# Optimization experiments

Measured on AMD Instinct MI355X. Metric: run time of the kernel, lower is better.

Reference implementation:

```python
import jax, jax.numpy as jnp
import numpy as np

NEG_FILL = -999999.0  # sentinel used by the original torch code when masking a channel


def setup_inputs() -> dict:
    key = jax.random.key(0)
    M = jax.random.normal(key, (64, 512, 28, 28), dtype=jnp.float32)
    return {"M": M}


def _dis_loss(M):
    # M: (b, c, h, w). Squared distance from each pixel to the per-map argmax, weighted by M.
    b, c, h, w = M.shape
    Mm = M.reshape(b * c, h, w)
    ind = jnp.argmax(Mm.reshape(b * c, h * w), axis=1)  # flat argmax per map
    indy = ind // w
    indx = ind % w
    y = jnp.arange(h)
    x = jnp.arange(w)
    dy2 = (indy[:, None, None] - y[None, :, None]) ** 2  # (bc, h, 1)
    dx2 = (indx[:, None, None] - x[None, None, :]) ** 2  # (bc, 1, w)
    dist_sq = (dy2 + dx2).astype(M.dtype)  # (bc, h, w)
    return jnp.mean(dist_sq * Mm)


def _div_loss(M):
    # Leave-one-out channel max times each channel, via a single top-2 over channels
    # (equivalent to the O(C^2) clone+max loop in the original).
    b, c, h, w = M.shape
    Mt = jnp.transpose(M, (0, 2, 3, 1))  # (b, h, w, c)
    vals, idxs = jax.lax.top_k(Mt, 2)    # (b, h, w, 2)
    ch = jnp.arange(c)
    # loo[..., c] = max over channels != c
    loo = jnp.where(ch[None, None, None, :] == idxs[..., :1], vals[..., 1:2], vals[..., :1])
    # Original caps the masked channel at -999999; only matters if all other channels < -999999.
    loo = jnp.maximum(loo, NEG_FILL)
    return jnp.mean(loo * Mt)


def reference(M):
    dis_loss = _dis_loss(M)
    div_loss = _div_loss(M)
    return (dis_loss, div_loss)
```

## Files before the change

### kernel.cpp

```cpp
#include <hip/hip_runtime.h>
#include <math.h>

#define BB 64
#define CC 512
#define HWP 784
#define NPIX4 12544
#define NCHUNK 16
#define NSLOTS 512
#define NEG_FILL -999999.0f
#define NTOT 25690112.0
#define PLANE_STRIDE 200704

static __device__ __forceinline__ unsigned sortable(float v) {
  unsigned b = __float_as_uint(v);
  return (b & 0x80000000u) ? ~b : (b | 0x80000000u);
}

static __device__ __forceinline__ void top2(float v, float& v1, float& v2) {
  float lo = fminf(v, v1);
  v1 = fmaxf(v1, v);
  v2 = fmaxf(v2, lo);
}

static __device__ __forceinline__ void mergev(float& v1, float& v2, float b1, float b2) {
  float lo = fminf(v1, b1);
  v1 = fmaxf(v1, b1);
  v2 = fmaxf(lo, fmaxf(v2, b2));
}
static __device__ __forceinline__ void mergev4(float4& v1, float4& v2, float4 b1, float4 b2) {
  mergev(v1.x, v2.x, b1.x, b2.x);
  mergev(v1.y, v2.y, b1.y, b2.y);
  mergev(v1.z, v2.z, b1.z, b2.z);
  mergev(v1.w, v2.w, b1.w, b2.w);
}

__global__ __launch_bounds__(256, 4) void fused_kernel(const float* __restrict__ M,
    double* __restrict__ slots, float4* __restrict__ wsV1,
    float4* __restrict__ wsV2, float4* __restrict__ wsS) {
  const int lane  = threadIdx.x & 63;
  const int w     = threadIdx.x >> 6;
  const int chunk = blockIdx.x;
  const int b     = blockIdx.y;
  const float* base = M + ((size_t)b * CC + chunk * 32 + w * 8) * HWP;

  float s0[8], sy[8], sx[8], bv[8];
  int bi[8];
  #pragma unroll
  for (int c = 0; c < 8; ++c) { s0[c]=0.f; sy[c]=0.f; sx[c]=0.f; bv[c]=-INFINITY; bi[c]=0; }
  float srr = 0.f;

  __shared__ float4 lm[4][3][196];

  auto process = [&](int f) {
    const int y  = f / 7;
    const int x0 = (f - y * 7) * 4;
    const float fy  = (float)y;
    const float fx0 = (float)x0, fx1 = fx0 + 1.f, fx2 = fx0 + 2.f, fx3 = fx0 + 3.f;
    const float fyy = fy * fy;
    const float rr0 = fyy + fx0*fx0, rr1 = fyy + fx1*fx1;
    const float rr2 = fyy + fx2*fx2, rr3 = fyy + fx3*fx3;
    const int pxb = f * 4;

    float4 d[8];
    #pragma unroll
    for (int c = 0; c < 8; ++c)
      d[c] = *(const float4*)(base + c * HWP + pxb);

    const float NI = -INFINITY;
    float4 v1 = make_float4(NI, NI, NI, NI);
    float4 v2 = v1;
    float4 S  = make_float4(0.f, 0.f, 0.f, 0.f);

    #pragma unroll
    for (int c = 0; c < 8; ++c) {
      const float a0 = d[c].x, a1 = d[c].y, a2 = d[c].z, a3 = d[c].w;
      const float sum4 = (a0 + a1) + (a2 + a3);
      s0[c] += sum4;
      sy[c] = fmaf(sum4, fy, sy[c]);
      sx[c] = fmaf(a0, fx0, sx[c]); sx[c] = fmaf(a1, fx1, sx[c]);
      sx[c] = fmaf(a2, fx2, sx[c]); sx[c] = fmaf(a3, fx3, sx[c]);
      srr = fmaf(a0, rr0, srr); srr = fmaf(a1, rr1, srr);
      srr = fmaf(a2, rr2, srr); srr = fmaf(a3, rr3, srr);
      if (a0 > bv[c]) { bv[c] = a0; bi[c] = pxb;     }
      if (a1 > bv[c]) { bv[c] = a1; bi[c] = pxb + 1; }
      if (a2 > bv[c]) { bv[c] = a2; bi[c] = pxb + 2; }
      if (a3 > bv[c]) { bv[c] = a3; bi[c] = pxb + 3; }
      top2(a0, v1.x, v2.x); S.x += a0;
      top2(a1, v1.y, v2.y); S.y += a1;
      top2(a2, v1.z, v2.z); S.z += a2;
      top2(a3, v1.w, v2.w); S.w += a3;
    }
    lm[w][0][f] = v1; lm[w][1][f] = v2; lm[w][2][f] = S;
  };

  #pragma unroll
  for (int k = 0; k < 3; ++k) process(lane + 64 * k);
  if (lane < 4) process(192 + lane);

  double dis_acc = (double)srr;
  #pragma unroll
  for (int c = 0; c < 8; ++c) {
    unsigned long long key =
        ((unsigned long long)sortable(bv[c]) << 32) | (unsigned)(~bi[c]);
    #pragma unroll
    for (int off = 1; off < 64; off <<= 1) {
      unsigned long long o = __shfl_xor(key, off);
      key = (key > o) ? key : o;
    }
    const int px = (int)(~((unsigned)key));
    const int iy = px / 28;
    const int ix = px - iy * 28;
    dis_acc += (double)s0[c] * (double)(iy * iy + ix * ix)
             - 2.0 * ((double)sy[c] * (double)iy + (double)sx[c] * (double)ix);
  }
  #pragma unroll
  for (int off = 32; off >= 1; off >>= 1)
    dis_acc += __shfl_down(dis_acc, off);
  if (lane == 0)
    atomicAdd(&slots[(((b * NCHUNK) + chunk) * 4 + w) & (NSLOTS - 1)], dis_acc);

  __syncthreads();
  const int t = threadIdx.x;
  if (t < 196) {
    float4 mv1 = lm[0][0][t], mv2 = lm[0][1][t], mS = lm[0][2][t];
    #pragma unroll
    for (int ww = 1; ww < 4; ++ww) {
      mergev4(mv1, mv2, lm[ww][0][t], lm[ww][1][t]);
      float4 bS = lm[ww][2][t];
      mS.x += bS.x; mS.y += bS.y; mS.z += bS.z; mS.w += bS.w;
    }
    const int idx = chunk * NPIX4 + b * 196 + t;
    wsV1[idx] = mv1; wsV2[idx] = mv2; wsS[idx] = mS;
  }
}

__global__ __launch_bounds__(256) void div_merge_kernel(const float4* __restrict__ wsV1,
    const float4* __restrict__ wsV2, const float4* __restrict__ wsS,
    double* __restrict__ slots) {
  const int t = threadIdx.x, lane = t & 63, w = t >> 6;
  const int g = blockIdx.x * 64 + lane;

  float4 a1[4], a2[4], aS[4];
  #pragma unroll
  for (int c = 0; c < 4; ++c) {
    const int idx = (w * 4 + c) * NPIX4 + g;
    a1[c] = wsV1[idx]; a2[c] = wsV2[idx]; aS[c] = wsS[idx];
  }
  float4 v1 = a1[0], v2 = a2[0], S = aS[0];
  #pragma unroll
  for (int c = 1; c < 4; ++c) {
    mergev4(v1, v2, a1[c], a2[c]);
    S.x += aS[c].x; S.y += aS[c].y; S.z += aS[c].z; S.w += aS[c].w;
  }
  __shared__ float4 sm[4][3][64];
  sm[w][0][lane] = v1; sm[w][1][lane] = v2; sm[w][2][lane] = S;
  __syncthreads();

  if (t < 64) {
    v1 = sm[0][0][t]; v2 = sm[0][1][t]; S = sm[0][2][t];
    #pragma unroll
    for (int ww = 1; ww < 4; ++ww) {
      mergev4(v1, v2, sm[ww][0][t], sm[ww][1][t]);
      float4 bS = sm[ww][2][t];
      S.x += bS.x; S.y += bS.y; S.z += bS.z; S.w += bS.w;
    }
    double contrib =
        (double)fmaxf(v1.x, NEG_FILL) * ((double)S.x - (double)v1.x) + (double)fmaxf(v2.x, NEG_FILL) * (double)v1.x
      + (double)fmaxf(v1.y, NEG_FILL) * ((double)S.y - (double)v1.y) + (double)fmaxf(v2.y, NEG_FILL) * (double)v1.y
      + (double)fmaxf(v1.z, NEG_FILL) * ((double)S.z - (double)v1.z) + (double)fmaxf(v2.z, NEG_FILL) * (double)v1.z
      + (double)fmaxf(v1.w, NEG_FILL) * ((double)S.w - (double)v1.w) + (double)fmaxf(v2.w, NEG_FILL) * (double)v1.w;
    #pragma unroll
    for (int off = 32; off >= 1; off >>= 1)
      contrib += __shfl_down(contrib, off);
    if (t == 0)
      atomicAdd(&slots[NSLOTS + blockIdx.x], contrib);
  }
}

__global__ __launch_bounds__(512) void finalize_kernel(const double* __restrict__ slots,
                                                       float* __restrict__ out) {
  const int t = threadIdx.x;
  const int lane = t & 63, wave = t >> 6;
  double dis = slots[t];
  double dv  = slots[NSLOTS + t];
  #pragma unroll
  for (int off = 32; off >= 1; off >>= 1) {
    dis += __shfl_down(dis, off);
    dv  += __shfl_down(dv,  off);
  }
  __shared__ double pd[8], pv[8];
  if (lane == 0) { pd[wave] = dis; pv[wave] = dv; }
  __syncthreads();
  if (t == 0) {
    double D = 0.0, V = 0.0;
    #pragma unroll
    for (int i = 0; i < 8; ++i) { D += pd[i]; V += pv[i]; }
    out[0] = (float)(D / NTOT);
    out[1] = (float)(V / NTOT);
  }
}

extern "C" void kernel_launch(void* const* d_in, const int* in_sizes, int n_in,
                              void* d_out, int out_size, void* d_ws, size_t ws_size,
                              hipStream_t stream) {
  const float* M = (const float*)d_in[0];
  double* slots = (double*)d_ws;
  float4* planes = (float4*)((char*)d_ws + 16384);
  hipMemsetAsync(d_ws, 0, 2 * NSLOTS * sizeof(double), stream);
  fused_kernel<<<dim3(NCHUNK, BB), 256, 0, stream>>>(
      M, slots, planes, planes + PLANE_STRIDE, planes + 2 * PLANE_STRIDE);
  div_merge_kernel<<<196, 256, 0, stream>>>(
      planes, planes + PLANE_STRIDE, planes + 2 * PLANE_STRIDE, slots);
  finalize_kernel<<<1, 512, 0, stream>>>(slots, (float*)d_out);
}
```

Measured before the change: 43.38 us.

## Use float2 loads with register double-buffering and drop atomics and memset

The main kernel now loads float2 instead of float4 per lane and software-pipelines the loads, fetching the next chunk of 8 channel rows into a second register set while the current one is processed. The tail is handled by a masked pass. The atomicAdd accumulation into hashed slots is replaced by a direct per-wave store into dedicated slots, which removes the hipMemsetAsync launch, and the finalize kernel sums the larger slot array. The intent is better memory-latency hiding and less launch and atomic overhead, at the cost of higher register pressure and more, smaller loads.

```diff
diff --git a/kernel.cpp b/kernel.cpp
--- a/kernel.cpp
+++ b/kernel.cpp
@@ -4,44 +4,40 @@
 #define BB 64
 #define CC 512
 #define HWP 784
+#define NF2 392
+#define NCHUNK 16
 #define NPIX4 12544
-#define NCHUNK 16
-#define NSLOTS 512
+#define NPIX2 25088
+#define PLANE2 401408
+#define DIS_SLOTS 4096
+#define DIV_SLOTS 196
 #define NEG_FILL -999999.0f
 #define NTOT 25690112.0
-#define PLANE_STRIDE 200704
 
 static __device__ __forceinline__ unsigned sortable(float v) {
   unsigned b = __float_as_uint(v);
   return (b & 0x80000000u) ? ~b : (b | 0x80000000u);
 }
-
 static __device__ __forceinline__ void top2(float v, float& v1, float& v2) {
   float lo = fminf(v, v1);
   v1 = fmaxf(v1, v);
   v2 = fmaxf(v2, lo);
 }
-
 static __device__ __forceinline__ void mergev(float& v1, float& v2, float b1, float b2) {
   float lo = fminf(v1, b1);
   v1 = fmaxf(v1, b1);
   v2 = fmaxf(lo, fmaxf(v2, b2));
 }
-static __device__ __forceinline__ void mergev4(float4& v1, float4& v2, float4 b1, float4 b2) {
-  mergev(v1.x, v2.x, b1.x, b2.x);
-  mergev(v1.y, v2.y, b1.y, b2.y);
-  mergev(v1.z, v2.z, b1.z, b2.z);
-  mergev(v1.w, v2.w, b1.w, b2.w);
-}
 
 __global__ __launch_bounds__(256, 4) void fused_kernel(const float* __restrict__ M,
-    double* __restrict__ slots, float4* __restrict__ wsV1,
-    float4* __restrict__ wsV2, float4* __restrict__ wsS) {
+    double* __restrict__ slots, float2* __restrict__ wsV1,
+    float2* __restrict__ wsV2, float2* __restrict__ wsS) {
   const int lane  = threadIdx.x & 63;
   const int w     = threadIdx.x >> 6;
   const int chunk = blockIdx.x;
   const int b     = blockIdx.y;
-  const float* base = M + ((size_t)b * CC + chunk * 32 + w * 8) * HWP;
+  const float2* base2 =
+      (const float2*)(M + ((size_t)b * CC + chunk * 32 + w * 8) * HWP);
 
   float s0[8], sy[8], sx[8], bv[8];
   int bi[8];
@@ -49,53 +45,58 @@
   for (int c = 0; c < 8; ++c) { s0[c]=0.f; sy[c]=0.f; sx[c]=0.f; bv[c]=-INFINITY; bi[c]=0; }
   float srr = 0.f;
 
-  __shared__ float4 lm[4][3][196];
-
-  auto process = [&](int f) {
-    const int y  = f / 7;
-    const int x0 = (f - y * 7) * 4;
+  __shared__ float2 lm[4][3][NF2];
+
+  float2 d[8], dn[8];
+  const int f2m = (lane < 8) ? (384 + lane) : 390;
+
+  #pragma unroll
+  for (int c = 0; c < 8; ++c) d[c] = base2[c * NF2 + lane];
+
+  auto consume = [&](int f2pos, bool masked) {
+    const int y  = f2pos / 14;
+    const int x0 = (f2pos - y * 14) * 2;
     const float fy  = (float)y;
-    const float fx0 = (float)x0, fx1 = fx0 + 1.f, fx2 = fx0 + 2.f, fx3 = fx0 + 3.f;
+    const float fx0 = (float)x0, fx1 = fx0 + 1.f;
     const float fyy = fy * fy;
-    const float rr0 = fyy + fx0*fx0, rr1 = fyy + fx1*fx1;
-    const float rr2 = fyy + fx2*fx2, rr3 = fyy + fx3*fx3;
-    const int pxb = f * 4;
-
-    float4 d[8];
-    #pragma unroll
-    for (int c = 0; c < 8; ++c)
-      d[c] = *(const float4*)(base + c * HWP + pxb);
-
-    const float NI = -INFINITY;
-    float4 v1 = make_float4(NI, NI, NI, NI);
-    float4 v2 = v1;
-    float4 S  = make_float4(0.f, 0.f, 0.f, 0.f);
-
+    const float rr0 = fyy + fx0 * fx0, rr1 = fyy + fx1 * fx1;
+    const int pxb = f2pos * 2;
+    const bool fake = masked && (lane >= 8);
+
+    float v1a = -INFINITY, v2a = -INFINITY, Sa = 0.f;
+    float v1b = -INFINITY, v2b = -INFINITY, Sb = 0.f;
     #pragma unroll
     for (int c = 0; c < 8; ++c) {
-      const float a0 = d[c].x, a1 = d[c].y, a2 = d[c].z, a3 = d[c].w;
-      const float sum4 = (a0 + a1) + (a2 + a3);
-      s0[c] += sum4;
-      sy[c] = fmaf(sum4, fy, sy[c]);
+      float a0 = d[c].x, a1 = d[c].y;
+      float c0 = a0,     c1 = a1;
+      if (masked && fake) { a0 = 0.f; a1 = 0.f; c0 = -INFINITY; c1 = -INFINITY; }
+      const float sum2 = a0 + a1;
+      s0[c] += sum2;
+      sy[c] = fmaf(sum2, fy, sy[c]);
       sx[c] = fmaf(a0, fx0, sx[c]); sx[c] = fmaf(a1, fx1, sx[c]);
-      sx[c] = fmaf(a2, fx2, sx[c]); sx[c] = fmaf(a3, fx3, sx[c]);
-      srr = fmaf(a0, rr0, srr); srr = fmaf(a1, rr1, srr);
-      srr = fmaf(a2, rr2, srr); srr = fmaf(a3, rr3, srr);
-      if (a0 > bv[c]) { bv[c] = a0; bi[c] = pxb;     }
-      if (a1 > bv[c]) { bv[c] = a1; bi[c] = pxb + 1; }
-      if (a2 > bv[c]) { bv[c] = a2; bi[c] = pxb + 2; }
-      if (a3 > bv[c]) { bv[c] = a3; bi[c] = pxb + 3; }
-      top2(a0, v1.x, v2.x); S.x += a0;
-      top2(a1, v1.y, v2.y); S.y += a1;
-      top2(a2, v1.z, v2.z); S.z += a2;
-      top2(a3, v1.w, v2.w); S.w += a3;
-    }
-    lm[w][0][f] = v1; lm[w][1][f] = v2; lm[w][2][f] = S;
+      srr   = fmaf(a0, rr0, srr);   srr   = fmaf(a1, rr1, srr);
+      if (c0 > bv[c]) { bv[c] = c0; bi[c] = pxb;     }
+      if (c1 > bv[c]) { bv[c] = c1; bi[c] = pxb + 1; }
+      top2(c0, v1a, v2a); Sa += a0;
+      top2(c1, v1b, v2b); Sb += a1;
+    }
+    if (!masked || lane < 8) {
+      lm[w][0][f2pos] = make_float2(v1a, v1b);
+      lm[w][1][f2pos] = make_float2(v2a, v2b);
+      lm[w][2][f2pos] = make_float2(Sa, Sb);
+    }
   };
 
   #pragma unroll
-  for (int k = 0; k < 3; ++k) process(lane + 64 * k);
-  if (lane < 4) process(192 + lane);
+  for (int k = 0; k < 6; ++k) {
+    const int nf2 = (k == 5) ? f2m : (lane + 64 * (k + 1));
+    #pragma unroll
+    for (int c = 0; c < 8; ++c) dn[c] = base2[c * NF2 + nf2];
+    consume(lane + 64 * k, false);
+    #pragma unroll
+    for (int c = 0; c < 8; ++c) d[c] = dn[c];
+  }
+  consume(384 + lane, true);
 
   double dis_acc = (double)srr;
   #pragma unroll
@@ -117,20 +118,25 @@
   for (int off = 32; off >= 1; off >>= 1)
     dis_acc += __shfl_down(dis_acc, off);
   if (lane == 0)
-    atomicAdd(&slots[(((b * NCHUNK) + chunk) * 4 + w) & (NSLOTS - 1)], dis_acc);
+    slots[((b * NCHUNK + chunk) << 2) | w] = dis_acc;
 
   __syncthreads();
   const int t = threadIdx.x;
-  if (t < 196) {
-    float4 mv1 = lm[0][0][t], mv2 = lm[0][1][t], mS = lm[0][2][t];
-    #pragma unroll
-    for (int ww = 1; ww < 4; ++ww) {
-      mergev4(mv1, mv2, lm[ww][0][t], lm[ww][1][t]);
-      float4 bS = lm[ww][2][t];
-      mS.x += bS.x; mS.y += bS.y; mS.z += bS.z; mS.w += bS.w;
-    }
-    const int idx = chunk * NPIX4 + b * 196 + t;
-    wsV1[idx] = mv1; wsV2[idx] = mv2; wsS[idx] = mS;
+  #pragma unroll
+  for (int rep = 0; rep < 2; ++rep) {
+    const int f = t + rep * 256;
+    if (f < NF2) {
+      float2 mv1 = lm[0][0][f], mv2 = lm[0][1][f], mS = lm[0][2][f];
+      #pragma unroll
+      for (int ww = 1; ww < 4; ++ww) {
+        float2 b1 = lm[ww][0][f], b2 = lm[ww][1][f], bS = lm[ww][2][f];
+        mergev(mv1.x, mv2.x, b1.x, b2.x);
+        mergev(mv1.y, mv2.y, b1.y, b2.y);
+        mS.x += bS.x; mS.y += bS.y;
+      }
+      const int idx = chunk * NPIX2 + b * NF2 + f;
+      wsV1[idx] = mv1; wsV2[idx] = mv2; wsS[idx] = mS;
+    }
   }
 }
 
@@ -149,7 +155,10 @@
   float4 v1 = a1[0], v2 = a2[0], S = aS[0];
   #pragma unroll
   for (int c = 1; c < 4; ++c) {
-    mergev4(v1, v2, a1[c], a2[c]);
+    mergev(v1.x, v2.x, a1[c].x, a2[c].x);
+    mergev(v1.y, v2.y, a1[c].y, a2[c].y);
+    mergev(v1.z, v2.z, a1[c].z, a2[c].z);
+    mergev(v1.w, v2.w, a1[c].w, a2[c].w);
     S.x += aS[c].x; S.y += aS[c].y; S.z += aS[c].z; S.w += aS[c].w;
   }
   __shared__ float4 sm[4][3][64];
@@ -160,7 +169,10 @@
     v1 = sm[0][0][t]; v2 = sm[0][1][t]; S = sm[0][2][t];
     #pragma unroll
     for (int ww = 1; ww < 4; ++ww) {
-      mergev4(v1, v2, sm[ww][0][t], sm[ww][1][t]);
+      mergev(v1.x, v2.x, sm[ww][0][t].x, sm[ww][1][t].x);
+      mergev(v1.y, v2.y, sm[ww][0][t].y, sm[ww][1][t].y);
+      mergev(v1.z, v2.z, sm[ww][0][t].z, sm[ww][1][t].z);
+      mergev(v1.w, v2.w, sm[ww][0][t].w, sm[ww][1][t].w);
       float4 bS = sm[ww][2][t];
       S.x += bS.x; S.y += bS.y; S.z += bS.z; S.w += bS.w;
     }
@@ -173,30 +185,28 @@
     for (int off = 32; off >= 1; off >>= 1)
       contrib += __shfl_down(contrib, off);
     if (t == 0)
-      atomicAdd(&slots[NSLOTS + blockIdx.x], contrib);
-  }
-}
-
-__global__ __launch_bounds__(512) void finalize_kernel(const double* __restrict__ slots,
+      slots[DIS_SLOTS + blockIdx.x] = contrib;
+  }
+}
+
+__global__ __launch_bounds__(256) void finalize_kernel(const double* __restrict__ slots,
                                                        float* __restrict__ out) {
-  const int t = threadIdx.x;
-  const int lane = t & 63, wave = t >> 6;
-  double dis = slots[t];
-  double dv  = slots[NSLOTS + t];
+  const int t = threadIdx.x, lane = t & 63, wv = t >> 6;
+  double dis = 0.0;
+  #pragma unroll
+  for (int i = 0; i < 16; ++i) dis += slots[t + (i << 8)];
+  double dv = (t < DIV_SLOTS) ? slots[DIS_SLOTS + t] : 0.0;
   #pragma unroll
   for (int off = 32; off >= 1; off >>= 1) {
     dis += __shfl_down(dis, off);
     dv  += __shfl_down(dv,  off);
   }
-  __shared__ double pd[8], pv[8];
-  if (lane == 0) { pd[wave] = dis; pv[wave] = dv; }
+  __shared__ double pd[4], pv[4];
+  if (lane == 0) { pd[wv] = dis; pv[wv] = dv; }
   __syncthreads();
   if (t == 0) {
-    double D = 0.0, V = 0.0;
-    #pragma unroll
-    for (int i = 0; i < 8; ++i) { D += pd[i]; V += pv[i]; }
-    out[0] = (float)(D / NTOT);
-    out[1] = (float)(V / NTOT);
+    out[0] = (float)((pd[0] + pd[1] + pd[2] + pd[3]) / NTOT);
+    out[1] = (float)((pv[0] + pv[1] + pv[2] + pv[3]) / NTOT);
   }
 }
 
@@ -205,11 +215,12 @@
                               hipStream_t stream) {
   const float* M = (const float*)d_in[0];
   double* slots = (double*)d_ws;
-  float4* planes = (float4*)((char*)d_ws + 16384);
-  hipMemsetAsync(d_ws, 0, 2 * NSLOTS * sizeof(double), stream);
-  fused_kernel<<<dim3(NCHUNK, BB), 256, 0, stream>>>(
-      M, slots, planes, planes + PLANE_STRIDE, planes + 2 * PLANE_STRIDE);
-  div_merge_kernel<<<196, 256, 0, stream>>>(
-      planes, planes + PLANE_STRIDE, planes + 2 * PLANE_STRIDE, slots);
-  finalize_kernel<<<1, 512, 0, stream>>>(slots, (float*)d_out);
-}
+  float2* planes = (float2*)((char*)d_ws + 65536);
+  float2* wsV1 = planes;
+  float2* wsV2 = planes + PLANE2;
+  float2* wsS  = planes + 2 * (size_t)PLANE2;
+  fused_kernel<<<dim3(NCHUNK, BB), 256, 0, stream>>>(M, slots, wsV1, wsV2, wsS);
+  div_merge_kernel<<<DIV_SLOTS, 256, 0, stream>>>(
+      (const float4*)wsV1, (const float4*)wsV2, (const float4*)wsS, slots);
+  finalize_kernel<<<1, 256, 0, stream>>>(slots, (float*)d_out);
+}
```

Result: slower. 45.56 us (+5.0%).

## Software-pipeline channel loads and fold finalize into merge via last-block ticket

Applied to the files above, without the earlier changes.

The main kernel now prefetches the next pixel group's channel data in two halves while computing the current one. The ragged tail lanes run the same code path with masked fake values, which removes divergence. The memset and the separate finalize kernel are gone: per-wave partials are written to unique slots instead of atomically added, and the last div_merge block, chosen by an atomic ticket counter, does the final reduction. This cuts two launches and adds more register pressure and a threadfence/atomic handshake.

```diff
diff --git a/kernel.cpp b/kernel.cpp
--- a/kernel.cpp
+++ b/kernel.cpp
@@ -4,24 +4,24 @@
 #define BB 64
 #define CC 512
 #define HWP 784
+#define NF4 196
+#define NCHUNK 16
 #define NPIX4 12544
-#define NCHUNK 16
-#define NSLOTS 512
+#define PLANE4 200704
+#define DIS_SLOTS 4096
+#define DIV_SLOTS 196
 #define NEG_FILL -999999.0f
 #define NTOT 25690112.0
-#define PLANE_STRIDE 200704
 
 static __device__ __forceinline__ unsigned sortable(float v) {
   unsigned b = __float_as_uint(v);
   return (b & 0x80000000u) ? ~b : (b | 0x80000000u);
 }
-
 static __device__ __forceinline__ void top2(float v, float& v1, float& v2) {
   float lo = fminf(v, v1);
   v1 = fmaxf(v1, v);
   v2 = fmaxf(v2, lo);
 }
-
 static __device__ __forceinline__ void mergev(float& v1, float& v2, float b1, float b2) {
   float lo = fminf(v1, b1);
   v1 = fmaxf(v1, b1);
@@ -34,14 +34,48 @@
   mergev(v1.w, v2.w, b1.w, b2.w);
 }
 
+#define CHBODY(c) {                                                          \
+    float a0 = d[c].x, a1 = d[c].y, a2 = d[c].z, a3 = d[c].w;                \
+    float q0 = a0, q1 = a1, q2 = a2, q3 = a3;                                \
+    if (fake) { a0 = a1 = a2 = a3 = 0.f;                                     \
+                q0 = q1 = q2 = q3 = -INFINITY; }                             \
+    const float sum4 = (a0 + a1) + (a2 + a3);                                \
+    s0[c] += sum4;                                                           \
+    sy[c] = fmaf(sum4, fy, sy[c]);                                           \
+    sx[c] = fmaf(a0, fx0, sx[c]); sx[c] = fmaf(a1, fx1, sx[c]);              \
+    sx[c] = fmaf(a2, fx2, sx[c]); sx[c] = fmaf(a3, fx3, sx[c]);              \
+    srr = fmaf(a0, rr0, srr); srr = fmaf(a1, rr1, srr);                      \
+    srr = fmaf(a2, rr2, srr); srr = fmaf(a3, rr3, srr);                      \
+    if (q0 > bv[c]) { bv[c] = q0; bi[c] = pxb;     }                         \
+    if (q1 > bv[c]) { bv[c] = q1; bi[c] = pxb + 1; }                         \
+    if (q2 > bv[c]) { bv[c] = q2; bi[c] = pxb + 2; }                         \
+    if (q3 > bv[c]) { bv[c] = q3; bi[c] = pxb + 3; }                         \
+    top2(q0, v1.x, v2.x); S.x += a0;                                         \
+    top2(q1, v1.y, v2.y); S.y += a1;                                         \
+    top2(q2, v1.z, v2.z); S.z += a2;                                         \
+    top2(q3, v1.w, v2.w); S.w += a3; }
+
+#define GEOM(f)                                                              \
+    const int y = (f) / 7;                                                   \
+    const float fy  = (float)y;                                              \
+    const float fx0 = (float)(((f) - y * 7) * 4);                            \
+    const float fx1 = fx0 + 1.f, fx2 = fx0 + 2.f, fx3 = fx0 + 3.f;           \
+    const float fyy = fy * fy;                                               \
+    const float rr0 = fyy + fx0 * fx0, rr1 = fyy + fx1 * fx1;                \
+    const float rr2 = fyy + fx2 * fx2, rr3 = fyy + fx3 * fx3;                \
+    const int pxb = (f) * 4;
+
 __global__ __launch_bounds__(256, 4) void fused_kernel(const float* __restrict__ M,
-    double* __restrict__ slots, float4* __restrict__ wsV1,
-    float4* __restrict__ wsV2, float4* __restrict__ wsS) {
+    double* __restrict__ slots, float4* __restrict__ wsV1, float4* __restrict__ wsV2,
+    float4* __restrict__ wsS, unsigned* __restrict__ counter) {
   const int lane  = threadIdx.x & 63;
   const int w     = threadIdx.x >> 6;
   const int chunk = blockIdx.x;
   const int b     = blockIdx.y;
-  const float* base = M + ((size_t)b * CC + chunk * 32 + w * 8) * HWP;
+  if (chunk == 0 && b == 0 && threadIdx.x == 0) *counter = 0u;
+
+  const float4* base4 =
+      (const float4*)(M + ((size_t)b * CC + chunk * 32 + w * 8) * HWP);
 
   float s0[8], sy[8], sx[8], bv[8];
   int bi[8];
@@ -49,53 +83,44 @@
   for (int c = 0; c < 8; ++c) { s0[c]=0.f; sy[c]=0.f; sx[c]=0.f; bv[c]=-INFINITY; bi[c]=0; }
   float srr = 0.f;
 
-  __shared__ float4 lm[4][3][196];
-
-  auto process = [&](int f) {
-    const int y  = f / 7;
-    const int x0 = (f - y * 7) * 4;
-    const float fy  = (float)y;
-    const float fx0 = (float)x0, fx1 = fx0 + 1.f, fx2 = fx0 + 2.f, fx3 = fx0 + 3.f;
-    const float fyy = fy * fy;
-    const float rr0 = fyy + fx0*fx0, rr1 = fyy + fx1*fx1;
-    const float rr2 = fyy + fx2*fx2, rr3 = fyy + fx3*fx3;
-    const int pxb = f * 4;
-
-    float4 d[8];
-    #pragma unroll
-    for (int c = 0; c < 8; ++c)
-      d[c] = *(const float4*)(base + c * HWP + pxb);
-
-    const float NI = -INFINITY;
-    float4 v1 = make_float4(NI, NI, NI, NI);
+  __shared__ float4 lm[4][3][NF4];
+
+  float4 d[8], dn[4];
+  #pragma unroll
+  for (int c = 0; c < 8; ++c) d[c] = base4[c * NF4 + lane];
+
+  const int tailf = (lane < 4) ? (192 + lane) : 195;
+
+  #pragma unroll
+  for (int k = 0; k < 3; ++k) {
+    const int f  = lane + 64 * k;
+    const int nf = (k == 2) ? tailf : (lane + 64 * (k + 1));
+    const bool fake = false;
+    GEOM(f)
+    float4 v1 = make_float4(-INFINITY, -INFINITY, -INFINITY, -INFINITY);
     float4 v2 = v1;
     float4 S  = make_float4(0.f, 0.f, 0.f, 0.f);
-
-    #pragma unroll
-    for (int c = 0; c < 8; ++c) {
-      const float a0 = d[c].x, a1 = d[c].y, a2 = d[c].z, a3 = d[c].w;
-      const float sum4 = (a0 + a1) + (a2 + a3);
-      s0[c] += sum4;
-      sy[c] = fmaf(sum4, fy, sy[c]);
-      sx[c] = fmaf(a0, fx0, sx[c]); sx[c] = fmaf(a1, fx1, sx[c]);
-      sx[c] = fmaf(a2, fx2, sx[c]); sx[c] = fmaf(a3, fx3, sx[c]);
-      srr = fmaf(a0, rr0, srr); srr = fmaf(a1, rr1, srr);
-      srr = fmaf(a2, rr2, srr); srr = fmaf(a3, rr3, srr);
-      if (a0 > bv[c]) { bv[c] = a0; bi[c] = pxb;     }
-      if (a1 > bv[c]) { bv[c] = a1; bi[c] = pxb + 1; }
-      if (a2 > bv[c]) { bv[c] = a2; bi[c] = pxb + 2; }
-      if (a3 > bv[c]) { bv[c] = a3; bi[c] = pxb + 3; }
-      top2(a0, v1.x, v2.x); S.x += a0;
-      top2(a1, v1.y, v2.y); S.y += a1;
-      top2(a2, v1.z, v2.z); S.z += a2;
-      top2(a3, v1.w, v2.w); S.w += a3;
-    }
+    #pragma unroll
+    for (int c = 0; c < 4; ++c) dn[c] = base4[c * NF4 + nf];
+    CHBODY(4) CHBODY(5) CHBODY(6) CHBODY(7)
+    #pragma unroll
+    for (int c = 4; c < 8; ++c) d[c] = base4[c * NF4 + nf];
+    CHBODY(0) CHBODY(1) CHBODY(2) CHBODY(3)
+    #pragma unroll
+    for (int c = 0; c < 4; ++c) d[c] = dn[c];
     lm[w][0][f] = v1; lm[w][1][f] = v2; lm[w][2][f] = S;
-  };
-
-  #pragma unroll
-  for (int k = 0; k < 3; ++k) process(lane + 64 * k);
-  if (lane < 4) process(192 + lane);
+  }
+  {
+    const int f = tailf;
+    const bool fake = (lane >= 4);
+    GEOM(f)
+    float4 v1 = make_float4(-INFINITY, -INFINITY, -INFINITY, -INFINITY);
+    float4 v2 = v1;
+    float4 S  = make_float4(0.f, 0.f, 0.f, 0.f);
+    CHBODY(0) CHBODY(1) CHBODY(2) CHBODY(3)
+    CHBODY(4) CHBODY(5) CHBODY(6) CHBODY(7)
+    if (!fake) { lm[w][0][f] = v1; lm[w][1][f] = v2; lm[w][2][f] = S; }
+  }
 
   double dis_acc = (double)srr;
   #pragma unroll
@@ -117,11 +142,11 @@
   for (int off = 32; off >= 1; off >>= 1)
     dis_acc += __shfl_down(dis_acc, off);
   if (lane == 0)
-    atomicAdd(&slots[(((b * NCHUNK) + chunk) * 4 + w) & (NSLOTS - 1)], dis_acc);
+    slots[((b * NCHUNK + chunk) << 2) | w] = dis_acc;
 
   __syncthreads();
   const int t = threadIdx.x;
-  if (t < 196) {
+  if (t < NF4) {
     float4 mv1 = lm[0][0][t], mv2 = lm[0][1][t], mS = lm[0][2][t];
     #pragma unroll
     for (int ww = 1; ww < 4; ++ww) {
@@ -129,14 +154,15 @@
       float4 bS = lm[ww][2][t];
       mS.x += bS.x; mS.y += bS.y; mS.z += bS.z; mS.w += bS.w;
     }
-    const int idx = chunk * NPIX4 + b * 196 + t;
+    const int idx = chunk * NPIX4 + b * NF4 + t;
     wsV1[idx] = mv1; wsV2[idx] = mv2; wsS[idx] = mS;
   }
 }
 
 __global__ __launch_bounds__(256) void div_merge_kernel(const float4* __restrict__ wsV1,
     const float4* __restrict__ wsV2, const float4* __restrict__ wsS,
-    double* __restrict__ slots) {
+    double* __restrict__ slots, unsigned* __restrict__ counter,
+    float* __restrict__ out) {
   const int t = threadIdx.x, lane = t & 63, w = t >> 6;
   const int g = blockIdx.x * 64 + lane;
 
@@ -173,30 +199,32 @@
     for (int off = 32; off >= 1; off >>= 1)
       contrib += __shfl_down(contrib, off);
     if (t == 0)
-      atomicAdd(&slots[NSLOTS + blockIdx.x], contrib);
-  }
-}
-
-__global__ __launch_bounds__(512) void finalize_kernel(const double* __restrict__ slots,
-                                                       float* __restrict__ out) {
-  const int t = threadIdx.x;
-  const int lane = t & 63, wave = t >> 6;
-  double dis = slots[t];
-  double dv  = slots[NSLOTS + t];
-  #pragma unroll
-  for (int off = 32; off >= 1; off >>= 1) {
-    dis += __shfl_down(dis, off);
-    dv  += __shfl_down(dv,  off);
-  }
-  __shared__ double pd[8], pv[8];
-  if (lane == 0) { pd[wave] = dis; pv[wave] = dv; }
-  __syncthreads();
-  if (t == 0) {
-    double D = 0.0, V = 0.0;
-    #pragma unroll
-    for (int i = 0; i < 8; ++i) { D += pd[i]; V += pv[i]; }
-    out[0] = (float)(D / NTOT);
-    out[1] = (float)(V / NTOT);
+      slots[DIS_SLOTS + blockIdx.x] = contrib;
+  }
+
+  __shared__ unsigned ticket_s;
+  __threadfence();
+  __syncthreads();
+  if (t == 0) ticket_s = atomicAdd(counter, 1u);
+  __syncthreads();
+  if (ticket_s == DIV_SLOTS - 1) {
+    __threadfence();
+    double dis = 0.0;
+    #pragma unroll
+    for (int i = 0; i < 16; ++i) dis += slots[t + (i << 8)];
+    double dv = (t < DIV_SLOTS) ? slots[DIS_SLOTS + t] : 0.0;
+    #pragma unroll
+    for (int off = 32; off >= 1; off >>= 1) {
+      dis += __shfl_down(dis, off);
+      dv  += __shfl_down(dv,  off);
+    }
+    __shared__ double pd[4], pv[4];
+    if (lane == 0) { pd[w] = dis; pv[w] = dv; }
+    __syncthreads();
+    if (t == 0) {
+      out[0] = (float)((pd[0] + pd[1] + pd[2] + pd[3]) / NTOT);
+      out[1] = (float)((pv[0] + pv[1] + pv[2] + pv[3]) / NTOT);
+    }
   }
 }
 
@@ -204,12 +232,13 @@
                               void* d_out, int out_size, void* d_ws, size_t ws_size,
                               hipStream_t stream) {
   const float* M = (const float*)d_in[0];
-  double* slots = (double*)d_ws;
-  float4* planes = (float4*)((char*)d_ws + 16384);
-  hipMemsetAsync(d_ws, 0, 2 * NSLOTS * sizeof(double), stream);
-  fused_kernel<<<dim3(NCHUNK, BB), 256, 0, stream>>>(
-      M, slots, planes, planes + PLANE_STRIDE, planes + 2 * PLANE_STRIDE);
-  div_merge_kernel<<<196, 256, 0, stream>>>(
-      planes, planes + PLANE_STRIDE, planes + 2 * PLANE_STRIDE, slots);
-  finalize_kernel<<<1, 512, 0, stream>>>(slots, (float*)d_out);
-}
+  double*   slots   = (double*)d_ws;
+  unsigned* counter = (unsigned*)((char*)d_ws + 40960);
+  float4*   planes  = (float4*)((char*)d_ws + 65536);
+  float4* wsV1 = planes;
+  float4* wsV2 = planes + PLANE4;
+  float4* wsS  = planes + 2 * (size_t)PLANE4;
+  fused_kernel<<<dim3(NCHUNK, BB), 256, 0, stream>>>(M, slots, wsV1, wsV2, wsS, counter);
+  div_merge_kernel<<<DIV_SLOTS, 256, 0, stream>>>(wsV1, wsV2, wsS, slots, counter,
+                                                  (float*)d_out);
+}
```

Measured after the change: 78.86 us. +81.8%, slower.
